# Kernel tuning notes

Hardware: AMD Instinct MI355X
Metric: run time of the kernel (lower is better)

The kernel has to match this reference:

```python
import jax, jax.numpy as jnp
import numpy as np
import math

N_EMBD = 1024
N_HEAD = 16
HEAD = N_EMBD // N_HEAD
LAMBDA_INIT = 0.8 - 0.6 * math.exp(-0.3 * (4 - 1))  # layer_idx=4
EPS = 1e-5


def setup_inputs() -> dict:
    key = jax.random.key(0)
    ks = jax.random.split(key, 12)
    s = 1.0 / math.sqrt(N_EMBD)
    inp = {
        "x": jax.random.normal(ks[0], (2, 2048, N_EMBD), dtype=jnp.float32),
        "q1_w": jax.random.normal(ks[1], (N_EMBD, N_EMBD), dtype=jnp.float32) * s,
        "q2_w": jax.random.normal(ks[2], (N_EMBD, N_EMBD), dtype=jnp.float32) * s,
        "k1_w": jax.random.normal(ks[3], (N_EMBD, N_EMBD), dtype=jnp.float32) * s,
        "k2_w": jax.random.normal(ks[4], (N_EMBD, N_EMBD), dtype=jnp.float32) * s,
        "v_w": jax.random.normal(ks[5], (N_EMBD, 2 * N_EMBD), dtype=jnp.float32) * s,
        "c_w": jax.random.normal(ks[6], (2 * N_EMBD, N_EMBD), dtype=jnp.float32) * (1.0 / math.sqrt(2 * N_EMBD)),
        "lambda_q1": jax.random.normal(ks[7], (N_HEAD, HEAD), dtype=jnp.float32) * 0.1,
        "lambda_k1": jax.random.normal(ks[8], (N_HEAD, HEAD), dtype=jnp.float32) * 0.1,
        "lambda_q2": jax.random.normal(ks[9], (N_HEAD, HEAD), dtype=jnp.float32) * 0.1,
        "lambda_k2": jax.random.normal(ks[10], (N_HEAD, HEAD), dtype=jnp.float32) * 0.1,
    }
    return inp


def reference(x, q1_w, q2_w, k1_w, k2_w, v_w, c_w,
              lambda_q1, lambda_k1, lambda_q2, lambda_k2):
    B, T, C = x.shape
    H, hs = N_HEAD, HEAD

    def heads(w, d):
        return (x @ w).reshape(B, T, H, d).transpose(0, 2, 1, 3)  # [B,H,T,d]

    q1 = heads(q1_w, hs)
    q2 = heads(q2_w, hs)
    k1 = heads(k1_w, hs)
    k2 = heads(k2_w, hs)
    v = heads(v_w, 2 * hs)  # [B,H,T,2*hs]

    scale = 1.0 / math.sqrt(hs)
    causal = jnp.tril(jnp.ones((T, T), dtype=bool))  # [T,T]
    neg = jnp.float32(-jnp.inf)

    att1 = jnp.einsum('bhqd,bhkd->bhqk', q1, k1) * scale
    att2 = jnp.einsum('bhqd,bhkd->bhqk', q2, k2) * scale
    att1 = jax.nn.softmax(jnp.where(causal, att1, neg), axis=-1)
    att2 = jax.nn.softmax(jnp.where(causal, att2, neg), axis=-1)

    lam1 = jnp.exp(jnp.sum(lambda_q1 * lambda_k1, axis=-1))  # [H]
    lam2 = jnp.exp(jnp.sum(lambda_q2 * lambda_k2, axis=-1))  # [H]
    lam = (lam1 - lam2 + LAMBDA_INIT)[None, :, None, None]

    att = att1 - lam * att2
    y = jnp.einsum('bhqk,bhkd->bhqd', att, v)  # [B,H,T,2*hs]

    # per-head LayerNorm over 2*hs, no affine
    mu = jnp.mean(y, axis=-1, keepdims=True)
    var = jnp.mean(jnp.square(y - mu), axis=-1, keepdims=True)
    y = (y - mu) / jnp.sqrt(var + EPS)
    y = y * (1.0 - LAMBDA_INIT)

    y = y.transpose(0, 2, 1, 3).reshape(B, T, 2 * C)
    return y @ c_w
```

## Files before the change

kernel.cpp:

```cpp
#include <hip/hip_runtime.h>
#include <cstdint>
#include <cstddef>

typedef __bf16 bf16;
typedef __bf16 bf16x8 __attribute__((ext_vector_type(8)));
typedef __bf16 bf16x4 __attribute__((ext_vector_type(4)));
typedef float f32x4 __attribute__((ext_vector_type(4)));

#define LAMBDA_INIT_F 0.5560582041556405f
#define ONE_MINUS_LI_F 0.4439417958443595f

static constexpr int T = 2048;
static constexpr int ROWQ = 6144;
#define C1_EXP2 0.18033688011116027f
#define C0_EXP2 -23.083120654223414f

__device__ __forceinline__ f32x4 mfma16(bf16x8 a, bf16x8 b, f32x4 c) {
  return __builtin_amdgcn_mfma_f32_16x16x32_bf16(a, b, c, 0, 0, 0);
}

__device__ __forceinline__ void gld16(const bf16* g, bf16* l) {
  __builtin_amdgcn_global_load_lds(
      (const __attribute__((address_space(1))) void*)g,
      (__attribute__((address_space(3))) void*)l, 16, 0, 0);
}


__global__ void cvt_f32_bf16(const float* __restrict__ src, bf16* __restrict__ dst, int n4) {
  int i = blockIdx.x * blockDim.x + threadIdx.x;
  if (i < n4) {
    float4 v = reinterpret_cast<const float4*>(src)[i];
    bf16x4 o;
    o[0] = (bf16)v.x; o[1] = (bf16)v.y; o[2] = (bf16)v.z; o[3] = (bf16)v.w;
    reinterpret_cast<bf16x4*>(dst)[i] = o;
  }
}

__global__ void transpose_all(const float* __restrict__ q1w, const float* __restrict__ q2w,
                              const float* __restrict__ k1w, const float* __restrict__ k2w,
                              const float* __restrict__ vw, const float* __restrict__ cw,
                              bf16* __restrict__ Wt, bf16* __restrict__ cwt) {
  __shared__ float t[32][33];
  const int id = blockIdx.x;
  const float* src;
  bf16* dst;
  int K, N, bx, by;
  if (id < 4096) {
    int wsel = id >> 10, r = id & 1023;
    src = (wsel == 0) ? q1w : (wsel == 1) ? q2w : (wsel == 2) ? k1w : k2w;
    dst = Wt + (size_t)wsel * 1024 * 1024;
    K = 1024; N = 1024; bx = r & 31; by = r >> 5;
  } else if (id < 6144) {
    int r = id - 4096;
    src = vw; dst = Wt + (size_t)4096 * 1024;
    K = 1024; N = 2048; bx = r & 63; by = r >> 6;
  } else {
    int r = id - 6144;
    src = cw; dst = cwt;
    K = 2048; N = 1024; bx = r & 31; by = r >> 5;
  }
  const int tx = threadIdx.x, ty = threadIdx.y;
  const int n0 = bx * 32, k0 = by * 32;
#pragma unroll
  for (int j = 0; j < 32; j += 8)
    t[ty + j][tx] = src[(size_t)(k0 + ty + j) * N + n0 + tx];
  __syncthreads();
#pragma unroll
  for (int j = 0; j < 32; j += 8)
    dst[(size_t)(n0 + ty + j) * K + k0 + tx] = (bf16)t[tx][ty + j];
}

__global__ void vtrans(const bf16* __restrict__ qkv, bf16* __restrict__ Vt) {
  __shared__ bf16 tile[64][72];
  const int tid = threadIdx.x;
  const int t0 = blockIdx.x * 64, dt = blockIdx.y, bh = blockIdx.z;
  const int b = bh >> 4, h = bh & 15;
#pragma unroll
  for (int i = 0; i < 2; ++i) {
    int S = tid + i * 256;
    int r = S >> 3, c = S & 7;
    *reinterpret_cast<bf16x8*>(&tile[r][c * 8]) =
        *reinterpret_cast<const bf16x8*>(
            &qkv[(size_t)(b * T + t0 + r) * ROWQ + 4096 + h * 128 + dt * 64 + c * 8]);
  }
  __syncthreads();
#pragma unroll
  for (int i = 0; i < 2; ++i) {
    int S = tid + i * 256;
    int dr = S >> 3, tc = S & 7;
    bf16x8 v;
#pragma unroll
    for (int j = 0; j < 8; ++j) v[j] = tile[tc * 8 + j][dr];
    *reinterpret_cast<bf16x8*>(
        &Vt[((size_t)bh * 128 + dt * 64 + dr) * 2048 + t0 + tc * 8]) = v;
  }
}


template <typename OutT, int BM>
__global__ __launch_bounds__(256, BM == 128 ? 2 : 3) void gemm_bt(
    const bf16* __restrict__ A, const bf16* __restrict__ Bt, OutT* __restrict__ C,
    int M, int N, int K) {
  constexpr int AIT = BM / 32;
  constexpr int AN = (BM == 128) ? 4 : 2;
  constexpr int WCN = (BM == 128) ? 64 : 32;
  __shared__ __align__(16) bf16 As[2][BM * 64];
  __shared__ __align__(16) bf16 Bs[2][128 * 64];
  const int tid = threadIdx.x;
  const int lane = tid & 63;
  const int wv = tid >> 6;
  const int wr = (BM == 128) ? (wv >> 1) : 0;
  const int wc = (BM == 128) ? (wv & 1) : wv;
  const int bm = blockIdx.y * BM, bn = blockIdx.x * 128;
  const int lr = lane & 15, lg = lane >> 4;

  f32x4 acc[4][AN] = {};
  const int KT = K >> 6;

#define STAGE_AB(buf, kk0)                                                      \
  do {                                                                          \
    _Pragma("unroll") for (int i_ = 0; i_ < 4; ++i_) {                          \
      int S_ = (i_ * 4 + wv) * 64 + lane;                                       \
      int rw_ = S_ >> 3;                                                        \
      int cg_ = (S_ & 7) ^ (rw_ & 7);                                           \
      if (i_ < AIT)                                                             \
        gld16(&A[(size_t)(bm + rw_) * K + (kk0) + cg_ * 8], &As[buf][(i_ * 4 + wv) * 512]); \
      gld16(&Bt[(size_t)(bn + rw_) * K + (kk0) + cg_ * 8], &Bs[buf][(i_ * 4 + wv) * 512]); \
    }                                                                           \
  } while (0)

  STAGE_AB(0, 0);
  for (int kt = 0; kt < KT; ++kt) {
    const int cur = kt & 1;
    asm volatile("s_waitcnt vmcnt(0)" ::: "memory");
    __syncthreads();
    if (kt + 1 < KT) STAGE_AB(cur ^ 1, (kt + 1) * 64);
#pragma unroll
    for (int kh = 0; kh < 2; ++kh) {
      bf16x8 af[4], bfr[AN];
#pragma unroll
      for (int m = 0; m < 4; ++m)
        af[m] = *reinterpret_cast<const bf16x8*>(
            &As[cur][(wr * 64 + m * 16 + lr) * 64 + (((kh * 4 + lg) ^ (lr & 7)) * 8)]);
#pragma unroll
      for (int n = 0; n < AN; ++n)
        bfr[n] = *reinterpret_cast<const bf16x8*>(
            &Bs[cur][(wc * WCN + n * 16 + lr) * 64 + (((kh * 4 + lg) ^ (lr & 7)) * 8)]);
#pragma unroll
      for (int m = 0; m < 4; ++m)
#pragma unroll
        for (int n = 0; n < AN; ++n)
          acc[m][n] = mfma16(af[m], bfr[n], acc[m][n]);
    }
  }
#undef STAGE_AB

#pragma unroll
  for (int m = 0; m < 4; ++m)
#pragma unroll
    for (int n = 0; n < AN; ++n)
#pragma unroll
      for (int r = 0; r < 4; ++r) {
        int row = bm + wr * 64 + m * 16 + lg * 4 + r;
        int col = bn + wc * WCN + n * 16 + lr;
        C[(size_t)row * N + col] = (OutT)acc[m][n][r];
      }
}


__global__ __launch_bounds__(256, 2) void diff_attn(const bf16* __restrict__ qkv,
                                                    const bf16* __restrict__ Vtg,
                                                    const float* __restrict__ lq1,
                                                    const float* __restrict__ lk1,
                                                    const float* __restrict__ lq2,
                                                    const float* __restrict__ lk2,
                                                    bf16* __restrict__ yln) {
  constexpr int LDP = 72;
  __shared__ __align__(16) bf16 K1s[2][64 * 64];
  __shared__ __align__(16) bf16 K2s[2][64 * 64];
  __shared__ __align__(16) bf16 Vs[2][128 * 64];
  __shared__ __align__(16) bf16 Ps[4][16 * LDP];

  const int x = blockIdx.x;
  const int bh = blockIdx.y;
  const int b = bh >> 4, h = bh & 15;
  const int tid = threadIdx.x, lane = tid & 63, wv = tid >> 6;
  const int lr = lane & 15, lg = lane >> 4;
  const int u = b ? x : 15 - x;
  const int qtA = 31 - u;
  const int qtB = u;

  const int q1c = h * 64;
  const int q2c = 1024 + h * 64;
  const int k1c = 2048 + h * 64;
  const int k2c = 3072 + h * 64;

  float a1 = lq1[h * 64 + lane] * lk1[h * 64 + lane];
  float a2 = lq2[h * 64 + lane] * lk2[h * 64 + lane];
#pragma unroll
  for (int m = 32; m >= 1; m >>= 1) {
    a1 += __shfl_xor(a1, m);
    a2 += __shfl_xor(a2, m);
  }
  const float lam = __expf(a1) - __expf(a2) + LAMBDA_INIT_F;

  bf16x8 onesf;
#pragma unroll
  for (int j = 0; j < 8; ++j) onesf[j] = (bf16)1.0f;

  bf16x8 q1fA[2], q2fA[2], q1fB[2], q2fB[2];
  {
    const bf16* qa = qkv + (size_t)(b * T + qtA * 64 + wv * 16 + lr) * ROWQ;
    const bf16* qb = qkv + (size_t)(b * T + qtB * 64 + wv * 16 + lr) * ROWQ;
#pragma unroll
    for (int kc = 0; kc < 2; ++kc) {
      q1fA[kc] = *reinterpret_cast<const bf16x8*>(qa + q1c + kc * 32 + lg * 8);
      q2fA[kc] = *reinterpret_cast<const bf16x8*>(qa + q2c + kc * 32 + lg * 8);
      q1fB[kc] = *reinterpret_cast<const bf16x8*>(qb + q1c + kc * 32 + lg * 8);
      q2fB[kc] = *reinterpret_cast<const bf16x8*>(qb + q2c + kc * 32 + lg * 8);
    }
  }

  f32x4 o1A[8] = {}, o2A[8] = {}, o1B[8] = {}, o2B[8] = {};
  f32x4 lA1 = {}, lA2 = {}, lB1 = {}, lB2 = {};

#define STAGE_KV(buf, tt0)                                                       \
  do {                                                                           \
    const bf16* kb_ = qkv + (size_t)(b * T + (tt0)) * ROWQ;                      \
    _Pragma("unroll") for (int i_ = 0; i_ < 2; ++i_) {                           \
      int S_ = (i_ * 4 + wv) * 64 + lane;                                        \
      int rw_ = S_ >> 3;                                                         \
      int cg_ = (S_ & 7) ^ (rw_ & 7);                                            \
      gld16(kb_ + (size_t)rw_ * ROWQ + k1c + cg_ * 8, &K1s[buf][(i_ * 4 + wv) * 512]); \
      gld16(kb_ + (size_t)rw_ * ROWQ + k2c + cg_ * 8, &K2s[buf][(i_ * 4 + wv) * 512]); \
    }                                                                            \
    _Pragma("unroll") for (int i_ = 0; i_ < 4; ++i_) {                           \
      int S_ = (i_ * 4 + wv) * 64 + lane;                                        \
      int dd_ = S_ >> 3;                                                         \
      int cg_ = (S_ & 7) ^ (dd_ & 7);                                            \
      gld16(Vtg + ((size_t)bh * 128 + dd_) * 2048 + (tt0) + cg_ * 8,             \
            &Vs[buf][(i_ * 4 + wv) * 512]);                                      \
    }                                                                            \
  } while (0)

#define ATT_STEP(q1f_, q2f_, o1_, o2_, l1_, l2_, edge_)                          \
  do {                                                                           \
    f32x4 s1_[4] = {}, s2_[4] = {};                                              \
    _Pragma("unroll") for (int n_ = 0; n_ < 4; ++n_) {                           \
      int krow_ = n_ * 16 + lr;                                                  \
      _Pragma("unroll") for (int kc_ = 0; kc_ < 2; ++kc_) {                      \
        bf16x8 kf1_ = *reinterpret_cast<const bf16x8*>(                          \
            &K1s[cur][krow_ * 64 + (((kc_ * 4 + lg) ^ (lr & 7)) * 8)]);          \
        bf16x8 kf2_ = *reinterpret_cast<const bf16x8*>(                          \
            &K2s[cur][krow_ * 64 + (((kc_ * 4 + lg) ^ (lr & 7)) * 8)]);          \
        s1_[n_] = mfma16(q1f_[kc_], kf1_, s1_[n_]);                              \
        s2_[n_] = mfma16(q2f_[kc_], kf2_, s2_[n_]);                              \
      }                                                                          \
    }                                                                            \
    _Pragma("unroll") for (int n_ = 0; n_ < 4; ++n_)                             \
    _Pragma("unroll") for (int r_ = 0; r_ < 4; ++r_) {                           \
      float e1_ = fmaf(s1_[n_][r_], C1_EXP2, C0_EXP2);                           \
      float e2_ = fmaf(s2_[n_][r_], C1_EXP2, C0_EXP2);                           \
      if (edge_) {                                                               \
        int qq_ = wv * 16 + lg * 4 + r_;                                         \
        int kk_ = n_ * 16 + lr;                                                  \
        if (kk_ > qq_) { e1_ = -10000.f; e2_ = -10000.f; }                       \
      }                                                                          \
      s1_[n_][r_] = exp2f(e1_);                                                  \
      s2_[n_][r_] = exp2f(e2_);                                                  \
    }                                                                            \
    bf16* Pw_ = &Ps[wv][0];                                                      \
    bf16x8 pa1_[2], pa2_[2];                                                     \
    _Pragma("unroll") for (int n_ = 0; n_ < 4; ++n_)                             \
    _Pragma("unroll") for (int r_ = 0; r_ < 4; ++r_)                             \
        Pw_[(lg * 4 + r_) * LDP + n_ * 16 + lr] = (bf16)s1_[n_][r_];             \
    _Pragma("unroll") for (int kc_ = 0; kc_ < 2; ++kc_)                          \
        pa1_[kc_] = *reinterpret_cast<const bf16x8*>(&Pw_[lr * LDP + kc_ * 32 + lg * 8]); \
    _Pragma("unroll") for (int n_ = 0; n_ < 4; ++n_)                             \
    _Pragma("unroll") for (int r_ = 0; r_ < 4; ++r_)                             \
        Pw_[(lg * 4 + r_) * LDP + n_ * 16 + lr] = (bf16)s2_[n_][r_];             \
    _Pragma("unroll") for (int kc_ = 0; kc_ < 2; ++kc_)                          \
        pa2_[kc_] = *reinterpret_cast<const bf16x8*>(&Pw_[lr * LDP + kc_ * 32 + lg * 8]); \
    _Pragma("unroll") for (int kc_ = 0; kc_ < 2; ++kc_) {                        \
      l1_ = mfma16(pa1_[kc_], onesf, l1_);                                       \
      l2_ = mfma16(pa2_[kc_], onesf, l2_);                                       \
      _Pragma("unroll") for (int nf_ = 0; nf_ < 8; ++nf_) {                      \
        int dd_ = nf_ * 16 + lr;                                                 \
        bf16x8 vb_ = *reinterpret_cast<const bf16x8*>(                           \
            &Vs[cur][dd_ * 64 + (((kc_ * 4 + lg) ^ (lr & 7)) * 8)]);             \
        o1_[nf_] = mfma16(pa1_[kc_], vb_, o1_[nf_]);                             \
        o2_[nf_] = mfma16(pa2_[kc_], vb_, o2_[nf_]);                             \
      }                                                                          \
    }                                                                            \
  } while (0)

  STAGE_KV(0, 0);
  for (int kt = 0; kt <= qtA; ++kt) {
    const int cur = kt & 1;
    asm volatile("s_waitcnt vmcnt(0)" ::: "memory");
    __syncthreads();
    if (kt < qtA) STAGE_KV(cur ^ 1, (kt + 1) * 64);
    __builtin_amdgcn_s_setprio(1);
    ATT_STEP(q1fA, q2fA, o1A, o2A, lA1, lA2, (kt == qtA));
    if (kt <= qtB) ATT_STEP(q1fB, q2fB, o1B, o2B, lB1, lB2, (kt == qtB));
    __builtin_amdgcn_s_setprio(0);
  }
#undef ATT_STEP
#undef STAGE_KV

#define ATT_EPI(o1_, o2_, l1_, l2_, qt_)                                         \
  do {                                                                           \
    float sum_[4] = {}, sq_[4] = {};                                             \
    float i1_[4], i2_[4];                                                        \
    _Pragma("unroll") for (int r_ = 0; r_ < 4; ++r_) {                           \
      i1_[r_] = 1.f / l1_[r_];                                                   \
      i2_[r_] = lam / l2_[r_];                                                   \
    }                                                                            \
    _Pragma("unroll") for (int nf_ = 0; nf_ < 8; ++nf_)                          \
    _Pragma("unroll") for (int r_ = 0; r_ < 4; ++r_) {                           \
      float v_ = o1_[nf_][r_] * i1_[r_] - o2_[nf_][r_] * i2_[r_];                \
      o1_[nf_][r_] = v_;                                                         \
      sum_[r_] += v_;                                                            \
      sq_[r_] += v_ * v_;                                                        \
    }                                                                            \
    _Pragma("unroll") for (int r_ = 0; r_ < 4; ++r_)                             \
    _Pragma("unroll") for (int mm_ = 8; mm_ >= 1; mm_ >>= 1) {                   \
      sum_[r_] += __shfl_xor(sum_[r_], mm_);                                     \
      sq_[r_] += __shfl_xor(sq_[r_], mm_);                                       \
    }                                                                            \
    _Pragma("unroll") for (int r_ = 0; r_ < 4; ++r_) {                           \
      float mu_ = sum_[r_] * (1.f / 128.f);                                      \
      float var_ = sq_[r_] * (1.f / 128.f) - mu_ * mu_;                          \
      float rs_ = rsqrtf(var_ + 1e-5f) * ONE_MINUS_LI_F;                         \
      int row_ = b * T + (qt_)*64 + wv * 16 + lg * 4 + r_;                       \
      bf16* orow_ = yln + (size_t)row_ * 2048 + h * 128;                         \
      _Pragma("unroll") for (int nf_ = 0; nf_ < 8; ++nf_)                        \
          orow_[nf_ * 16 + lr] = (bf16)((o1_[nf_][r_] - mu_) * rs_);             \
    }                                                                            \
  } while (0)

  ATT_EPI(o1A, o2A, lA1, lA2, qtA);
  ATT_EPI(o1B, o2B, lB1, lB2, qtB);
#undef ATT_EPI
}


extern "C" void kernel_launch(void* const* d_in, const int* in_sizes, int n_in,
                              void* d_out, int out_size, void* d_ws, size_t ws_size,
                              hipStream_t stream) {
  const float* x   = (const float*)d_in[0];
  const float* q1w = (const float*)d_in[1];
  const float* q2w = (const float*)d_in[2];
  const float* k1w = (const float*)d_in[3];
  const float* k2w = (const float*)d_in[4];
  const float* vw  = (const float*)d_in[5];
  const float* cw  = (const float*)d_in[6];
  const float* lq1 = (const float*)d_in[7];
  const float* lk1 = (const float*)d_in[8];
  const float* lq2 = (const float*)d_in[9];
  const float* lk2 = (const float*)d_in[10];
  float* out = (float*)d_out;

  char* ws = (char*)d_ws;
  bf16* qkv = (bf16*)(ws);
  bf16* Wt  = (bf16*)(ws + 50331648);
  bf16* xb  = (bf16*)(ws + 62914560);
  bf16* cwt = (bf16*)(ws + 71303168);
  bf16* yln = (bf16*)(ws + 75497472);
  bf16* Vt  = (bf16*)(ws + 50331648);

  cvt_f32_bf16<<<4096, 256, 0, stream>>>(x, xb, 4096 * 1024 / 4);

  transpose_all<<<8192, dim3(32, 8), 0, stream>>>(q1w, q2w, k1w, k2w, vw, cw, Wt, cwt);

  gemm_bt<bf16, 128><<<dim3(48, 32), 256, 0, stream>>>(xb, Wt, qkv, 4096, 6144, 1024);

  vtrans<<<dim3(32, 2, 32), 256, 0, stream>>>(qkv, Vt);

  diff_attn<<<dim3(16, 32), 256, 0, stream>>>(qkv, Vt, lq1, lk1, lq2, lk2, yln);

  gemm_bt<float, 64><<<dim3(8, 64), 256, 0, stream>>>(yln, cwt, out, 4096, 1024, 2048);
}
```

Before: 219.3 us.

## Fuse V transpose into QKV GEMM epilogue and drop explicit vmcnt waits

When the workspace is large enough, the QKV GEMM now writes the V columns straight into the transposed Vt layout. It does this through a shared-memory staging tile in the epilogue, which removes the separate vtrans kernel and its extra read and write of V. The explicit s_waitcnt vmcnt(0) before each barrier and the setprio hints in the attention loop are also removed. The attention step moves from a macro into an inline function, with exp2 replaced by an equivalent __expf form. The fused path depends on the runtime workspace size. Dropping the explicit waits relies on the barrier to order the async LDS loads, which carries a correctness risk.

```diff
diff --git a/kernel.cpp b/kernel.cpp
--- a/kernel.cpp
+++ b/kernel.cpp
@@ -12,8 +12,6 @@
 
 static constexpr int T = 2048;
 static constexpr int ROWQ = 6144;
-#define C1_EXP2 0.18033688011116027f
-#define C0_EXP2 -23.083120654223414f
 
 __device__ __forceinline__ f32x4 mfma16(bf16x8 a, bf16x8 b, f32x4 c) {
   return __builtin_amdgcn_mfma_f32_16x16x32_bf16(a, b, c, 0, 0, 0);
@@ -97,15 +95,14 @@
 }
 
 
-template <typename OutT, int BM>
+template <typename OutT, int BM, bool FUSEV>
 __global__ __launch_bounds__(256, BM == 128 ? 2 : 3) void gemm_bt(
     const bf16* __restrict__ A, const bf16* __restrict__ Bt, OutT* __restrict__ C,
-    int M, int N, int K) {
+    bf16* __restrict__ Vt, int M, int N, int K) {
   constexpr int AIT = BM / 32;
   constexpr int AN = (BM == 128) ? 4 : 2;
   constexpr int WCN = (BM == 128) ? 64 : 32;
-  __shared__ __align__(16) bf16 As[2][BM * 64];
-  __shared__ __align__(16) bf16 Bs[2][128 * 64];
+  __shared__ __align__(16) bf16 smem[2 * BM * 64 + 2 * 128 * 64];
   const int tid = threadIdx.x;
   const int lane = tid & 63;
   const int wv = tid >> 6;
@@ -117,6 +114,9 @@
   f32x4 acc[4][AN] = {};
   const int KT = K >> 6;
 
+#define ASB(buf) (smem + (buf) * (BM * 64))
+#define BSB(buf) (smem + 2 * BM * 64 + (buf) * (128 * 64))
+
 #define STAGE_AB(buf, kk0)                                                      \
   do {                                                                          \
     _Pragma("unroll") for (int i_ = 0; i_ < 4; ++i_) {                          \
@@ -124,15 +124,14 @@
       int rw_ = S_ >> 3;                                                        \
       int cg_ = (S_ & 7) ^ (rw_ & 7);                                           \
       if (i_ < AIT)                                                             \
-        gld16(&A[(size_t)(bm + rw_) * K + (kk0) + cg_ * 8], &As[buf][(i_ * 4 + wv) * 512]); \
-      gld16(&Bt[(size_t)(bn + rw_) * K + (kk0) + cg_ * 8], &Bs[buf][(i_ * 4 + wv) * 512]); \
+        gld16(&A[(size_t)(bm + rw_) * K + (kk0) + cg_ * 8], ASB(buf) + (i_ * 4 + wv) * 512); \
+      gld16(&Bt[(size_t)(bn + rw_) * K + (kk0) + cg_ * 8], BSB(buf) + (i_ * 4 + wv) * 512); \
     }                                                                           \
   } while (0)
 
   STAGE_AB(0, 0);
   for (int kt = 0; kt < KT; ++kt) {
     const int cur = kt & 1;
-    asm volatile("s_waitcnt vmcnt(0)" ::: "memory");
     __syncthreads();
     if (kt + 1 < KT) STAGE_AB(cur ^ 1, (kt + 1) * 64);
 #pragma unroll
@@ -141,11 +140,11 @@
 #pragma unroll
       for (int m = 0; m < 4; ++m)
         af[m] = *reinterpret_cast<const bf16x8*>(
-            &As[cur][(wr * 64 + m * 16 + lr) * 64 + (((kh * 4 + lg) ^ (lr & 7)) * 8)]);
+            ASB(cur) + (wr * 64 + m * 16 + lr) * 64 + (((kh * 4 + lg) ^ (lr & 7)) * 8));
 #pragma unroll
       for (int n = 0; n < AN; ++n)
         bfr[n] = *reinterpret_cast<const bf16x8*>(
-            &Bs[cur][(wc * WCN + n * 16 + lr) * 64 + (((kh * 4 + lg) ^ (lr & 7)) * 8)]);
+            BSB(cur) + (wc * WCN + n * 16 + lr) * 64 + (((kh * 4 + lg) ^ (lr & 7)) * 8));
 #pragma unroll
       for (int m = 0; m < 4; ++m)
 #pragma unroll
@@ -154,19 +153,118 @@
     }
   }
 #undef STAGE_AB
-
-#pragma unroll
-  for (int m = 0; m < 4; ++m)
-#pragma unroll
-    for (int n = 0; n < AN; ++n)
-#pragma unroll
-      for (int r = 0; r < 4; ++r) {
-        int row = bm + wr * 64 + m * 16 + lg * 4 + r;
-        int col = bn + wc * WCN + n * 16 + lr;
-        C[(size_t)row * N + col] = (OutT)acc[m][n][r];
+#undef ASB
+#undef BSB
+
+  bool vpath = false;
+  if constexpr (FUSEV) vpath = (bn >= 4096);
+  if (!vpath) {
+#pragma unroll
+    for (int m = 0; m < 4; ++m)
+#pragma unroll
+      for (int n = 0; n < AN; ++n)
+#pragma unroll
+        for (int r = 0; r < 4; ++r) {
+          int row = bm + wr * 64 + m * 16 + lg * 4 + r;
+          int col = bn + wc * WCN + n * 16 + lr;
+          C[(size_t)row * N + col] = (OutT)acc[m][n][r];
+        }
+  } else if constexpr (FUSEV) {
+    constexpr int LDT = 136;
+    bf16* tb = smem;
+    __syncthreads();
+#pragma unroll
+    for (int m = 0; m < 4; ++m)
+#pragma unroll
+      for (int n = 0; n < AN; ++n) {
+        int dl = wc * WCN + n * 16 + lr;
+        int tl = wr * 64 + m * 16 + lg * 4;
+        bf16x4 p;
+#pragma unroll
+        for (int r = 0; r < 4; ++r) p[r] = (bf16)acc[m][n][r];
+        *reinterpret_cast<bf16x4*>(&tb[dl * LDT + tl]) = p;
       }
-}
-
+    __syncthreads();
+    const int b_ = bm >> 11;
+    const int t0g = bm & 2047;
+    const int h_ = (bn - 4096) >> 7;
+#pragma unroll
+    for (int i = 0; i < 8; ++i) {
+      int S = i * 256 + tid;
+      int dl = S >> 4, tc = S & 15;
+      bf16x8 v = *reinterpret_cast<const bf16x8*>(&tb[dl * LDT + tc * 8]);
+      *reinterpret_cast<bf16x8*>(
+          &Vt[(((size_t)b_ * 16 + h_) * 128 + dl) * 2048 + t0g + tc * 8]) = v;
+    }
+  }
+}
+
+
+__device__ __forceinline__ void att_step(
+    const bf16* __restrict__ K1c, const bf16* __restrict__ K2c,
+    const bf16* __restrict__ Vc, bf16* __restrict__ Pw,
+    const bf16x8 (&q1f)[2], const bf16x8 (&q2f)[2],
+    f32x4 (&o1)[8], f32x4 (&o2)[8], f32x4& l1, f32x4& l2,
+    bool edge, int lr, int lg, int wv, const bf16x8& onesf) {
+  constexpr int LDP = 72;
+  f32x4 s1[4] = {}, s2[4] = {};
+#pragma unroll
+  for (int n = 0; n < 4; ++n) {
+    int krow = n * 16 + lr;
+#pragma unroll
+    for (int kc = 0; kc < 2; ++kc) {
+      int off = krow * 64 + (((kc * 4 + lg) ^ (lr & 7)) * 8);
+      bf16x8 kf1 = *reinterpret_cast<const bf16x8*>(&K1c[off]);
+      bf16x8 kf2 = *reinterpret_cast<const bf16x8*>(&K2c[off]);
+      s1[n] = mfma16(q1f[kc], kf1, s1[n]);
+      s2[n] = mfma16(q2f[kc], kf2, s2[n]);
+    }
+  }
+#pragma unroll
+  for (int n = 0; n < 4; ++n)
+#pragma unroll
+    for (int r = 0; r < 4; ++r) {
+      float e1 = fmaf(s1[n][r], 0.125f, -16.0f);
+      float e2 = fmaf(s2[n][r], 0.125f, -16.0f);
+      if (edge) {
+        int qq = wv * 16 + lg * 4 + r;
+        int kk = n * 16 + lr;
+        if (kk > qq) { e1 = -10000.f; e2 = -10000.f; }
+      }
+      s1[n][r] = __expf(e1);
+      s2[n][r] = __expf(e2);
+    }
+  bf16x8 pa1[2], pa2[2];
+#pragma unroll
+  for (int n = 0; n < 4; ++n)
+#pragma unroll
+    for (int r = 0; r < 4; ++r)
+      Pw[(lg * 4 + r) * LDP + n * 16 + lr] = (bf16)s1[n][r];
+#pragma unroll
+  for (int kc = 0; kc < 2; ++kc)
+    pa1[kc] = *reinterpret_cast<const bf16x8*>(&Pw[lr * LDP + kc * 32 + lg * 8]);
+#pragma unroll
+  for (int n = 0; n < 4; ++n)
+#pragma unroll
+    for (int r = 0; r < 4; ++r)
+      Pw[(lg * 4 + r) * LDP + n * 16 + lr] = (bf16)s2[n][r];
+#pragma unroll
+  for (int kc = 0; kc < 2; ++kc)
+    pa2[kc] = *reinterpret_cast<const bf16x8*>(&Pw[lr * LDP + kc * 32 + lg * 8]);
+#pragma unroll
+  for (int kc = 0; kc < 2; ++kc) {
+    l1 = mfma16(pa1[kc], onesf, l1);
+    l2 = mfma16(pa2[kc], onesf, l2);
+#pragma unroll
+    for (int nf = 0; nf < 8; ++nf) {
+      int dd = nf * 16 + lr;
+      int off = dd * 64 + (((kc * 4 + lg) ^ (lr & 7)) * 8);
+      bf16x8 vb = *reinterpret_cast<const bf16x8*>(&Vc[off]);
+      o1[nf] = mfma16(pa1[kc], vb, o1[nf]);
+      o2[nf] = mfma16(pa2[kc], vb, o2[nf]);
+    }
+  }
+}
 
 __global__ __launch_bounds__(256, 2) void diff_attn(const bf16* __restrict__ qkv,
                                                     const bf16* __restrict__ Vtg,
@@ -243,69 +341,17 @@
     }                                                                            \
   } while (0)
 
-#define ATT_STEP(q1f_, q2f_, o1_, o2_, l1_, l2_, edge_)                          \
-  do {                                                                           \
-    f32x4 s1_[4] = {}, s2_[4] = {};                                              \
-    _Pragma("unroll") for (int n_ = 0; n_ < 4; ++n_) {                           \
-      int krow_ = n_ * 16 + lr;                                                  \
-      _Pragma("unroll") for (int kc_ = 0; kc_ < 2; ++kc_) {                      \
-        bf16x8 kf1_ = *reinterpret_cast<const bf16x8*>(                          \
-            &K1s[cur][krow_ * 64 + (((kc_ * 4 + lg) ^ (lr & 7)) * 8)]);          \
-        bf16x8 kf2_ = *reinterpret_cast<const bf16x8*>(                          \
-            &K2s[cur][krow_ * 64 + (((kc_ * 4 + lg) ^ (lr & 7)) * 8)]);          \
-        s1_[n_] = mfma16(q1f_[kc_], kf1_, s1_[n_]);                              \
-        s2_[n_] = mfma16(q2f_[kc_], kf2_, s2_[n_]);                              \
-      }                                                                          \
-    }                                                                            \
-    _Pragma("unroll") for (int n_ = 0; n_ < 4; ++n_)                             \
-    _Pragma("unroll") for (int r_ = 0; r_ < 4; ++r_) {                           \
-      float e1_ = fmaf(s1_[n_][r_], C1_EXP2, C0_EXP2);                           \
-      float e2_ = fmaf(s2_[n_][r_], C1_EXP2, C0_EXP2);                           \
-      if (edge_) {                                                               \
-        int qq_ = wv * 16 + lg * 4 + r_;                                         \
-        int kk_ = n_ * 16 + lr;                                                  \
-        if (kk_ > qq_) { e1_ = -10000.f; e2_ = -10000.f; }                       \
-      }                                                                          \
-      s1_[n_][r_] = exp2f(e1_);                                                  \
-      s2_[n_][r_] = exp2f(e2_);                                                  \
-    }                                                                            \
-    bf16* Pw_ = &Ps[wv][0];                                                      \
-    bf16x8 pa1_[2], pa2_[2];                                                     \
-    _Pragma("unroll") for (int n_ = 0; n_ < 4; ++n_)                             \
-    _Pragma("unroll") for (int r_ = 0; r_ < 4; ++r_)                             \
-        Pw_[(lg * 4 + r_) * LDP + n_ * 16 + lr] = (bf16)s1_[n_][r_];             \
-    _Pragma("unroll") for (int kc_ = 0; kc_ < 2; ++kc_)                          \
-        pa1_[kc_] = *reinterpret_cast<const bf16x8*>(&Pw_[lr * LDP + kc_ * 32 + lg * 8]); \
-    _Pragma("unroll") for (int n_ = 0; n_ < 4; ++n_)                             \
-    _Pragma("unroll") for (int r_ = 0; r_ < 4; ++r_)                             \
-        Pw_[(lg * 4 + r_) * LDP + n_ * 16 + lr] = (bf16)s2_[n_][r_];             \
-    _Pragma("unroll") for (int kc_ = 0; kc_ < 2; ++kc_)                          \
-        pa2_[kc_] = *reinterpret_cast<const bf16x8*>(&Pw_[lr * LDP + kc_ * 32 + lg * 8]); \
-    _Pragma("unroll") for (int kc_ = 0; kc_ < 2; ++kc_) {                        \
-      l1_ = mfma16(pa1_[kc_], onesf, l1_);                                       \
-      l2_ = mfma16(pa2_[kc_], onesf, l2_);                                       \
-      _Pragma("unroll") for (int nf_ = 0; nf_ < 8; ++nf_) {                      \
-        int dd_ = nf_ * 16 + lr;                                                 \
-        bf16x8 vb_ = *reinterpret_cast<const bf16x8*>(                           \
-            &Vs[cur][dd_ * 64 + (((kc_ * 4 + lg) ^ (lr & 7)) * 8)]);             \
-        o1_[nf_] = mfma16(pa1_[kc_], vb_, o1_[nf_]);                             \
-        o2_[nf_] = mfma16(pa2_[kc_], vb_, o2_[nf_]);                             \
-      }                                                                          \
-    }                                                                            \
-  } while (0)
-
   STAGE_KV(0, 0);
   for (int kt = 0; kt <= qtA; ++kt) {
     const int cur = kt & 1;
-    asm volatile("s_waitcnt vmcnt(0)" ::: "memory");
     __syncthreads();
     if (kt < qtA) STAGE_KV(cur ^ 1, (kt + 1) * 64);
-    __builtin_amdgcn_s_setprio(1);
-    ATT_STEP(q1fA, q2fA, o1A, o2A, lA1, lA2, (kt == qtA));
-    if (kt <= qtB) ATT_STEP(q1fB, q2fB, o1B, o2B, lB1, lB2, (kt == qtB));
-    __builtin_amdgcn_s_setprio(0);
-  }
-#undef ATT_STEP
+    att_step(&K1s[cur][0], &K2s[cur][0], &Vs[cur][0], &Ps[wv][0], q1fA, q2fA,
+             o1A, o2A, lA1, lA2, kt == qtA, lr, lg, wv, onesf);
+    if (kt <= qtB)
+      att_step(&K1s[cur][0], &K2s[cur][0], &Vs[cur][0], &Ps[wv][0], q1fB, q2fB,
+               o1B, o2B, lB1, lB2, kt == qtB, lr, lg, wv, onesf);
+  }
 #undef STAGE_KV
 
 #define ATT_EPI(o1_, o2_, l1_, l2_, qt_)                                         \
@@ -367,17 +413,22 @@
   bf16* xb  = (bf16*)(ws + 62914560);
   bf16* cwt = (bf16*)(ws + 71303168);
   bf16* yln = (bf16*)(ws + 75497472);
-  bf16* Vt  = (bf16*)(ws + 50331648);
+
+  const bool fuse_v = (ws_size >= 92274688ull + 16777216ull);
+  bf16* Vt = fuse_v ? (bf16*)(ws + 92274688) : (bf16*)(ws + 50331648);
 
   cvt_f32_bf16<<<4096, 256, 0, stream>>>(x, xb, 4096 * 1024 / 4);
 
   transpose_all<<<8192, dim3(32, 8), 0, stream>>>(q1w, q2w, k1w, k2w, vw, cw, Wt, cwt);
 
-  gemm_bt<bf16, 128><<<dim3(48, 32), 256, 0, stream>>>(xb, Wt, qkv, 4096, 6144, 1024);
-
-  vtrans<<<dim3(32, 2, 32), 256, 0, stream>>>(qkv, Vt);
+  if (fuse_v) {
+    gemm_bt<bf16, 128, true><<<dim3(48, 32), 256, 0, stream>>>(xb, Wt, qkv, Vt, 4096, 6144, 1024);
+  } else {
+    gemm_bt<bf16, 128, false><<<dim3(48, 32), 256, 0, stream>>>(xb, Wt, qkv, nullptr, 4096, 6144, 1024);
+    vtrans<<<dim3(32, 2, 32), 256, 0, stream>>>(qkv, Vt);
+  }
 
   diff_attn<<<dim3(16, 32), 256, 0, stream>>>(qkv, Vt, lq1, lk1, lq2, lk2, yln);
 
-  gemm_bt<float, 64><<<dim3(8, 64), 256, 0, stream>>>(yln, cwt, out, 4096, 1024, 2048);
-}
+  gemm_bt<float, 64, false><<<dim3(8, 64), 256, 0, stream>>>(yln, cwt, out, nullptr, 4096, 1024, 2048);
+}
```

New measurement: 304.7 us. +39.0%, slower.
